# Performance work log

Measured on AMD Instinct MI355X. Metric: run time of the kernel, lower is better.

Reference implementation:

```python
import jax, jax.numpy as jnp
import numpy as np

N_NODES = 100000
N_EDGES = 3200000
N_GRAPHS = 64
NEG_SLOPE = 0.2


def mish(x):
    return x * jnp.tanh(jax.nn.softplus(x))


def gat_layer(x, src, dst, W, b, a_src, a_dst, heads, out_ch, n_nodes):
    # h: [N, H, C]
    h = (x @ W).reshape(n_nodes, heads, out_ch)
    alpha_s = jnp.sum(h * a_src[None], axis=-1)  # [N, H]
    alpha_d = jnp.sum(h * a_dst[None], axis=-1)  # [N, H]
    e = jax.nn.leaky_relu(alpha_s[src] + alpha_d[dst], NEG_SLOPE)  # [E, H]
    # scatter-softmax over incoming edges of each destination node
    emax = jax.ops.segment_max(e, dst, num_segments=n_nodes)  # [N, H]
    ee = jnp.exp(e - emax[dst])
    den = jax.ops.segment_sum(ee, dst, num_segments=n_nodes)
    alpha = ee / (den[dst] + 1e-16)  # [E, H]
    msg = h[src] * alpha[..., None]  # [E, H, C]
    out = jax.ops.segment_sum(msg, dst, num_segments=n_nodes)
    return out.reshape(n_nodes, heads * out_ch) + b


def setup_inputs() -> dict:
    key = jax.random.key(0)
    ks = jax.random.split(key, 10)
    x = jax.random.normal(ks[0], (N_NODES, 128), dtype=jnp.float32)
    edge_index = jax.random.randint(ks[1], (2, N_EDGES), 0, N_NODES, dtype=jnp.int64)
    batch = jnp.sort(jax.random.randint(ks[2], (N_NODES,), 0, N_GRAPHS, dtype=jnp.int64))
    s1 = 1.0 / np.sqrt(128.0)
    s2 = 1.0 / np.sqrt(16.0)
    return {
        "x": x,
        "edge_index": edge_index,
        "batch": batch,
        "W1": jax.random.normal(ks[3], (128, 16), dtype=jnp.float32) * s1,
        "b1": jnp.zeros((16,), dtype=jnp.float32),
        "a_src1": jax.random.normal(ks[4], (4, 4), dtype=jnp.float32) * 0.5,
        "a_dst1": jax.random.normal(ks[5], (4, 4), dtype=jnp.float32) * 0.5,
        "W2": jax.random.normal(ks[6], (16, 32), dtype=jnp.float32) * s2,
        "b2": jnp.zeros((32,), dtype=jnp.float32),
        "a_src2": jax.random.normal(ks[7], (1, 32), dtype=jnp.float32) * 0.5,
        "a_dst2": jax.random.normal(ks[8], (1, 32), dtype=jnp.float32) * 0.5,
    }


def reference(x, edge_index, batch, W1, b1, a_src1, a_dst1, W2, b2, a_src2, a_dst2):
    n = x.shape[0]
    # PyG GATConv default add_self_loops=True
    loop = jnp.arange(n, dtype=edge_index.dtype)
    src = jnp.concatenate([edge_index[0], loop])
    dst = jnp.concatenate([edge_index[1], loop])
    h = mish(gat_layer(x, src, dst, W1, b1, a_src1, a_dst1, heads=4, out_ch=4, n_nodes=n))
    h = mish(gat_layer(h, src, dst, W2, b2, a_src2, a_dst2, heads=1, out_ch=32, n_nodes=n))
    # global_mean_pool
    sums = jax.ops.segment_sum(h, batch, num_segments=N_GRAPHS)
    cnts = jax.ops.segment_sum(jnp.ones((n,), h.dtype), batch, num_segments=N_GRAPHS)
    return sums / jnp.maximum(cnts, 1.0)[:, None]
```

## Files before the change

kernel.cpp:

```cpp
#include <hip/hip_runtime.h>
#include <hip/hip_fp16.h>
#include <math.h>

#define NEG_SLOPE 0.2f
#define SB 256
#define NBMAX 1024
#define CAP 5120

typedef _Float16 half2v __attribute__((ext_vector_type(2)));

__device__ __forceinline__ float mishf(float x) {
    if (x > 15.f) return x;
    float ex = __expf(x);
    float y = 1.f + ex;
    float y2 = y * y;
    return x * (y2 - 1.f) / (y2 + 1.f);
}

__device__ __forceinline__ float lw(float e) {
    return __expf(fmaxf(e, NEG_SLOPE * e));
}

__device__ __forceinline__ float hdot2(half2v a, half2v b) {
#if __has_builtin(__builtin_amdgcn_fdot2)
    return __builtin_amdgcn_fdot2(a, b, 0.f, false);
#else
    return (float)a.x * (float)b.x + (float)a.y * (float)b.y;
#endif
}

__global__ void gemm1_kernel(const float* __restrict__ x, const float* __restrict__ W1,
                             const float* __restrict__ a_dst,
                             const float* __restrict__ W2, const float* __restrict__ as2,
                             const float* __restrict__ ad2,
                             _Float16* __restrict__ hpre1h, float* __restrict__ addst,
                             int* __restrict__ cursor, float* __restrict__ pool,
                             float* __restrict__ cnt, float* __restrict__ vs,
                             float* __restrict__ vd, int NB, int NG, int N) {
    __shared__ float Wl[128 * 16];
    __shared__ float xs[16 * 132];
    int tid = threadIdx.x;
    if (blockIdx.x == 0) {
        for (int i = tid; i < NB; i += 256) cursor[i] = 0;
        for (int i = tid; i < NG * 32; i += 256) pool[i] = 0.f;
        for (int i = tid; i < NG; i += 256) cnt[i] = 0.f;
        if (tid < 16) {
            float ps = 0.f, pd = 0.f;
            #pragma unroll
            for (int c = 0; c < 32; c++) {
                float w = W2[tid * 32 + c];
                ps += w * as2[c];
                pd += w * ad2[c];
            }
            vs[tid] = ps; vd[tid] = pd;
        }
    }
    for (int i = tid; i < 2048; i += 256) Wl[i] = W1[i];
    int nodebase = blockIdx.x * 16;
    const float4* x4 = (const float4*)(x + (size_t)nodebase * 128);
    for (int i = tid; i < 512; i += 256) {
        float4 v = x4[i];
        int e = i * 4;
        int nl = e >> 7, k = e & 127;
        float* dp = &xs[nl * 132 + k];
        dp[0] = v.x; dp[1] = v.y; dp[2] = v.z; dp[3] = v.w;
    }
    __syncthreads();
    int nl = tid >> 4, ch = tid & 15;
    const float* xr = &xs[nl * 132];
    float acc = 0.f;
    #pragma unroll 8
    for (int k = 0; k < 128; k++) acc += xr[k] * Wl[k * 16 + ch];
    int node = nodebase + nl;
    if (node < N) {
        hpre1h[node * 16 + ch] = (_Float16)acc;
        float pd = acc * a_dst[ch];
        pd += __shfl_xor(pd, 1); pd += __shfl_xor(pd, 2);
        if ((ch & 3) == 0) addst[node * 4 + (ch >> 2)] = pd;
    }
}

__global__ __launch_bounds__(1024) void scatF_kernel(
        const int* __restrict__ src, const int* __restrict__ dst,
        int E, int Etot, int CH, int NB,
        int* __restrict__ cursor, int* __restrict__ pairs) {
    __shared__ int lcnt[NBMAX];
    __shared__ int lbase[NBMAX];
    int tid = threadIdx.x, blk = blockIdx.x;
    for (int b = tid; b < NB; b += 1024) lcnt[b] = 0;
    __syncthreads();
    int ibeg = blk * CH, iend = min((blk + 1) * CH, Etot);
    for (int i = ibeg + tid; i < iend; i += 1024) {
        int d = (i < E) ? dst[i] : (i - E);
        atomicAdd(&lcnt[d >> 7], 1);
    }
    __syncthreads();
    for (int b = tid; b < NB; b += 1024) {
        int h = lcnt[b];
        lbase[b] = h ? atomicAdd(&cursor[b], h) : 0;
    }
    __syncthreads();
    for (int b = tid; b < NB; b += 1024) lcnt[b] = 0;
    __syncthreads();
    for (int i = ibeg + tid; i < iend; i += 1024) {
        int s, d;
        if (i < E) { s = src[i]; d = dst[i]; } else { s = d = i - E; }
        int b = d >> 7, dl = d & 127;
        int r = atomicAdd(&lcnt[b], 1);
        int pos = lbase[b] + r;
        pairs[(size_t)b * CAP + (pos < CAP ? pos : CAP - 1)] = s | (dl << 17);
    }
}

__global__ __launch_bounds__(1024) void csragg1_kernel(
        const int* __restrict__ pairs, const int* __restrict__ btotal,
        int NB, int N,
        int* __restrict__ ssorted, int* __restrict__ rs, int* __restrict__ re,
        const float* __restrict__ a_src1, const float* __restrict__ addst,
        const _Float16* __restrict__ hpre1h, const float* __restrict__ b1,
        const float* __restrict__ vs, const float* __restrict__ vd,
        _Float16* __restrict__ hpost1h,
        float* __restrict__ as2n, float* __restrict__ ad2n) {
    __shared__ int deg[128];
    __shared__ int s[128];
    __shared__ int cur[128];
    int tid = threadIdx.x, b = blockIdx.x;
    int nb0 = b << 7;
    int cnt_nodes = min(128, N - nb0);
    int bstart = b * CAP;
    int bend = bstart + btotal[b];
    if (tid < 128) deg[tid] = 0;
    __syncthreads();
    for (int j = bstart + tid; j < bend; j += 1024)
        atomicAdd(&deg[(pairs[j] >> 17) & 127], 1);
    __syncthreads();
    if (tid < 128) s[tid] = deg[tid];
    __syncthreads();
    for (int o = 1; o < 128; o <<= 1) {
        int v = 0;
        if (tid < 128 && tid >= o) v = s[tid - o];
        __syncthreads();
        if (tid < 128) s[tid] += v;
        __syncthreads();
    }
    if (tid < 128) {
        int ex = bstart + s[tid] - deg[tid];
        cur[tid] = ex;
        if (tid < cnt_nodes) {
            rs[nb0 + tid] = ex;
            re[nb0 + tid] = ex + deg[tid];
        }
    }
    __syncthreads();
    for (int j = bstart + tid; j < bend; j += 1024) {
        int p = pairs[j];
        int pos = atomicAdd(&cur[(p >> 17) & 127], 1);
        ssorted[pos] = p & 0x1FFFF;
    }
    __syncthreads();

    int wave = tid >> 6;
    int lane = tid & 63;
    int er = lane >> 3, hc = lane & 7, head = hc >> 1;
    int c0 = hc * 2;
    half2v wsh;
    wsh.x = (_Float16)a_src1[c0];
    wsh.y = (_Float16)a_src1[c0 + 1];
    const _Float16* hb = hpre1h + c0;
    for (int r = 0; r < 8; r++) {
        int ln = (wave << 3) + r;
        if (ln >= cnt_nodes) break;
        int node = nb0 + ln;
        int end = cur[ln];
        int start = end - deg[ln];
        float adh = addst[node * 4 + head];
        float den = 0.f, a0 = 0.f, a1 = 0.f;
        int last = end - 1;
        int jb = start;
        for (; jb + 16 <= end; jb += 16) {
            int j0 = jb + er, j1 = j0 + 8;
            int s0 = ssorted[j0];
            int s1 = ssorted[j1];
            half2v h0 = *(const half2v*)(hb + s0 * 16);
            half2v h1 = *(const half2v*)(hb + s1 * 16);
            float p0 = hdot2(h0, wsh);
            float p1 = hdot2(h1, wsh);
            float w0 = lw(p0 + __shfl_xor(p0, 1) + adh);
            float w1 = lw(p1 + __shfl_xor(p1, 1) + adh);
            den += w0 + w1;
            a0 += (float)h0.x * w0 + (float)h1.x * w1;
            a1 += (float)h0.y * w0 + (float)h1.y * w1;
        }
        if (jb < end) {
            int j0 = jb + er, j1 = j0 + 8;
            int k0 = (j0 <= last) ? j0 : last;
            int k1 = (j1 <= last) ? j1 : last;
            int s0 = ssorted[k0];
            int s1 = ssorted[k1];
            half2v h0 = *(const half2v*)(hb + s0 * 16);
            half2v h1 = *(const half2v*)(hb + s1 * 16);
            float p0 = hdot2(h0, wsh);
            float p1 = hdot2(h1, wsh);
            float e0 = p0 + __shfl_xor(p0, 1) + adh;
            float e1 = p1 + __shfl_xor(p1, 1) + adh;
            float w0 = (j0 <= last) ? lw(e0) : 0.f;
            float w1 = (j1 <= last) ? lw(e1) : 0.f;
            den += w0 + w1;
            a0 += (float)h0.x * w0 + (float)h1.x * w1;
            a1 += (float)h0.y * w0 + (float)h1.y * w1;
        }
        a0 += __shfl_xor(a0, 8);  a1 += __shfl_xor(a1, 8);  den += __shfl_xor(den, 8);
        a0 += __shfl_xor(a0, 16); a1 += __shfl_xor(a1, 16); den += __shfl_xor(den, 16);
        a0 += __shfl_xor(a0, 32); a1 += __shfl_xor(a1, 32); den += __shfl_xor(den, 32);
        if (er == 0) {
            float inv = 1.f / (den + 1e-16f);
            float o0 = mishf(a0 * inv + b1[c0]);
            float o1 = mishf(a1 * inv + b1[c0 + 1]);
            half2v oh;
            oh.x = (_Float16)o0; oh.y = (_Float16)o1;
            *(half2v*)(hpost1h + node * 16 + c0) = oh;
            float ps = o0 * vs[c0] + o1 * vs[c0 + 1];
            float pd = o0 * vd[c0] + o1 * vd[c0 + 1];
            ps += __shfl_xor(ps, 1); pd += __shfl_xor(pd, 1);
            ps += __shfl_xor(ps, 2); pd += __shfl_xor(pd, 2);
            ps += __shfl_xor(ps, 4); pd += __shfl_xor(pd, 4);
            if (hc == 0) { as2n[node] = ps; ad2n[node] = pd; }
        }
    }
}

__global__ void agg2_kernel(const int* __restrict__ rs, const int* __restrict__ re,
                            const int* __restrict__ ssorted,
                            const float* __restrict__ as2n, const float* __restrict__ ad2n,
                            const _Float16* __restrict__ hpost1h,
                            float* __restrict__ agg16, float* __restrict__ denv, int N) {
    int wave = threadIdx.x >> 6;
    int lane = threadIdx.x & 63;
    int node = blockIdx.x * 4 + wave;
    if (node >= N) return;
    int start = rs[node], end = re[node];
    int er = lane >> 3, hc = lane & 7;
    int c0 = hc * 2;
    float adh = ad2n[node];
    const _Float16* hb = hpost1h + c0;
    float den = 0.f, a0 = 0.f, a1 = 0.f;
    int last = end - 1;
    int jb = start;
    for (; jb + 16 <= end; jb += 16) {
        int j0 = jb + er, j1 = j0 + 8;
        int s0 = __builtin_nontemporal_load(ssorted + j0);
        int s1 = __builtin_nontemporal_load(ssorted + j1);
        float e0 = as2n[s0] + adh;
        float e1 = as2n[s1] + adh;
        half2v h0 = *(const half2v*)(hb + s0 * 16);
        half2v h1 = *(const half2v*)(hb + s1 * 16);
        float w0 = lw(e0);
        float w1 = lw(e1);
        den += w0 + w1;
        a0 += (float)h0.x * w0 + (float)h1.x * w1;
        a1 += (float)h0.y * w0 + (float)h1.y * w1;
    }
    if (jb < end) {
        int j0 = jb + er, j1 = j0 + 8;
        int k0 = (j0 <= last) ? j0 : last;
        int k1 = (j1 <= last) ? j1 : last;
        int s0 = __builtin_nontemporal_load(ssorted + k0);
        int s1 = __builtin_nontemporal_load(ssorted + k1);
        float e0 = as2n[s0] + adh;
        float e1 = as2n[s1] + adh;
        half2v h0 = *(const half2v*)(hb + s0 * 16);
        half2v h1 = *(const half2v*)(hb + s1 * 16);
        float w0 = (j0 <= last) ? lw(e0) : 0.f;
        float w1 = (j1 <= last) ? lw(e1) : 0.f;
        den += w0 + w1;
        a0 += (float)h0.x * w0 + (float)h1.x * w1;
        a1 += (float)h0.y * w0 + (float)h1.y * w1;
    }
    a0 += __shfl_xor(a0, 8);  a1 += __shfl_xor(a1, 8);  den += __shfl_xor(den, 8);
    a0 += __shfl_xor(a0, 16); a1 += __shfl_xor(a1, 16); den += __shfl_xor(den, 16);
    a0 += __shfl_xor(a0, 32); a1 += __shfl_xor(a1, 32); den += __shfl_xor(den, 32);
    if (er == 0) {
        float2 o; o.x = a0; o.y = a1;
        *(float2*)(agg16 + node * 16 + c0) = o;
        if (hc == 0) denv[node] = den;
    }
}

__global__ void post2pool_kernel(const float* __restrict__ agg16, const float* __restrict__ denv,
                                 const float* __restrict__ W2, const float* __restrict__ b2,
                                 const int* __restrict__ batch,
                                 float* __restrict__ pool, float* __restrict__ cnt, int N) {
    __shared__ float Wl[16 * 32];
    int tid = threadIdx.x;
    for (int i = tid; i < 512; i += 256) Wl[i] = W2[i];
    __syncthreads();
    int r = tid >> 5, ch = tid & 31;
    float bc = b2[ch];
    int base = blockIdx.x * 512;
    int cur = -1;
    float sum = 0.f, c = 0.f;
    for (int it = 0; it < 64; it++) {
        int n = base + it * 8 + r;
        if (n >= N) break;
        int g = batch[n];
        if (g != cur) {
            if (cur >= 0) {
                atomicAdd(&pool[cur * 32 + ch], sum);
                if (ch == 0) atomicAdd(&cnt[cur], c);
            }
            cur = g; sum = 0.f; c = 0.f;
        }
        const float* ar = agg16 + (size_t)n * 16;
        float acc = 0.f;
        #pragma unroll
        for (int k = 0; k < 16; k++) acc += ar[k] * Wl[k * 32 + ch];
        float val = mishf(acc / (denv[n] + 1e-16f) + bc);
        sum += val;
        c += 1.f;
    }
    if (cur >= 0) {
        atomicAdd(&pool[cur * 32 + ch], sum);
        if (ch == 0) atomicAdd(&cnt[cur], c);
    }
}

__global__ void fin_kernel(const float* __restrict__ pool, const float* __restrict__ cnt,
                           float* __restrict__ out, int NG) {
    int i = blockIdx.x * blockDim.x + threadIdx.x;
    if (i >= NG * 32) return;
    out[i] = pool[i] / fmaxf(cnt[i >> 5], 1.0f);
}

extern "C" void kernel_launch(void* const* d_in, const int* in_sizes, int n_in,
                              void* d_out, int out_size, void* d_ws, size_t ws_size,
                              hipStream_t stream) {
    const float* x   = (const float*)d_in[0];
    const int* eidx  = (const int*)d_in[1];
    const int* batch = (const int*)d_in[2];
    const float* W1  = (const float*)d_in[3];
    const float* b1  = (const float*)d_in[4];
    const float* as1 = (const float*)d_in[5];
    const float* ad1 = (const float*)d_in[6];
    const float* W2  = (const float*)d_in[7];
    const float* b2  = (const float*)d_in[8];
    const float* as2 = (const float*)d_in[9];
    const float* ad2 = (const float*)d_in[10];
    float* out = (float*)d_out;

    int N = in_sizes[0] / 128;
    int E = in_sizes[1] / 2;
    int Etot = E + N;
    int NG = out_size / 32;
    const int* esrc = eidx;
    const int* edst = eidx + E;

    int NB = (N + 127) >> 7;
    int CH = (Etot + SB - 1) / SB;

    char* p = (char*)d_ws;
    auto alloc = [&](size_t nbytes) {
        p = (char*)(((uintptr_t)p + 15) & ~(uintptr_t)15);
        void* r = (void*)p; p += nbytes; return r;
    };
    int* pairs        = (int*)alloc((size_t)NB * CAP * 4);
    int* ssorted      = (int*)alloc((size_t)NB * CAP * 4);
    int* rs           = (int*)alloc((size_t)N * 4);
    int* re           = (int*)alloc((size_t)N * 4);
    int* cursor       = (int*)alloc((size_t)NB * 4);
    _Float16* hpre1h  = (_Float16*)alloc((size_t)N * 16 * 2);
    _Float16* hpost1h = (_Float16*)alloc((size_t)N * 16 * 2);
    float* addst1  = (float*)alloc((size_t)N * 4 * 4);
    float* as2n    = (float*)alloc((size_t)N * 4);
    float* ad2n    = (float*)alloc((size_t)N * 4);
    float* agg16   = (float*)alloc((size_t)N * 16 * 4);
    float* denv    = (float*)alloc((size_t)N * 4);
    float* vs      = (float*)alloc(16 * 4);
    float* vd      = (float*)alloc(16 * 4);
    float* pool    = (float*)alloc((size_t)NG * 32 * 4);
    float* cnt     = (float*)alloc((size_t)NG * 4);

    gemm1_kernel<<<(N + 15) / 16, 256, 0, stream>>>(x, W1, ad1, W2, as2, ad2,
                                                    hpre1h, addst1, cursor, pool, cnt,
                                                    vs, vd, NB, NG, N);
    scatF_kernel<<<SB, 1024, 0, stream>>>(esrc, edst, E, Etot, CH, NB, cursor, pairs);
    csragg1_kernel<<<NB, 1024, 0, stream>>>(pairs, cursor, NB, N,
                                            ssorted, rs, re, as1, addst1, hpre1h,
                                            b1, vs, vd, hpost1h, as2n, ad2n);
    agg2_kernel<<<(N + 3) / 4, 256, 0, stream>>>(rs, re, ssorted, as2n, ad2n, hpost1h,
                                                 agg16, denv, N);
    post2pool_kernel<<<(N + 511) / 512, 256, 0, stream>>>(agg16, denv, W2, b2, batch,
                                                          pool, cnt, N);
    fin_kernel<<<(NG * 32 + 255) / 256, 256, 0, stream>>>(pool, cnt, out, NG);
}
```

Baseline: 349.9 us.

## Merge GEMM1 and edge bucketing into one launch; stage sorted sources in LDS

Combines the layer-1 projection GEMM and the edge bucket-scatter into a single kernel whose blocks are split by block index, so the two independent stages can run concurrently. The scatter moves from 256 blocks of 1024 threads to 1024 blocks of 256. Zeroing of cursor, pool and count buffers moves to a single hipMemsetAsync over contiguously allocated buffers. The CSR aggregation kernel now keeps the per-bucket sorted source list in shared memory and reads it from there during aggregation, which adds 20 KB of LDS per block and may reduce occupancy.

```diff
diff --git a/kernel.cpp b/kernel.cpp
--- a/kernel.cpp
+++ b/kernel.cpp
@@ -3,7 +3,7 @@
 #include <math.h>
 
 #define NEG_SLOPE 0.2f
-#define SB 256
+#define SCB 1024
 #define NBMAX 1024
 #define CAP 5120
 
@@ -29,22 +29,50 @@
 #endif
 }
 
-__global__ void gemm1_kernel(const float* __restrict__ x, const float* __restrict__ W1,
-                             const float* __restrict__ a_dst,
-                             const float* __restrict__ W2, const float* __restrict__ as2,
-                             const float* __restrict__ ad2,
-                             _Float16* __restrict__ hpre1h, float* __restrict__ addst,
-                             int* __restrict__ cursor, float* __restrict__ pool,
-                             float* __restrict__ cnt, float* __restrict__ vs,
-                             float* __restrict__ vd, int NB, int NG, int N) {
-    __shared__ float Wl[128 * 16];
-    __shared__ float xs[16 * 132];
+__global__ __launch_bounds__(256) void gemm1scat_kernel(
+        const float* __restrict__ x, const float* __restrict__ W1,
+        const float* __restrict__ a_dst,
+        const float* __restrict__ W2, const float* __restrict__ as2,
+        const float* __restrict__ ad2,
+        _Float16* __restrict__ hpre1h, float* __restrict__ addst,
+        const int* __restrict__ src, const int* __restrict__ dst,
+        int E, int Etot, int CH, int NB,
+        int* __restrict__ cursor, int* __restrict__ pairs,
+        float* __restrict__ vs, float* __restrict__ vd,
+        int G1, int N) {
+    __shared__ char smem[16640];
     int tid = threadIdx.x;
-    if (blockIdx.x == 0) {
-        for (int i = tid; i < NB; i += 256) cursor[i] = 0;
-        for (int i = tid; i < NG * 32; i += 256) pool[i] = 0.f;
-        for (int i = tid; i < NG; i += 256) cnt[i] = 0.f;
-        if (tid < 16) {
+    if ((int)blockIdx.x < G1) {
+        float* Wl = (float*)smem;
+        float* xs = (float*)(smem + 8192);
+        for (int i = tid; i < 2048; i += 256) Wl[i] = W1[i];
+        int nodebase = blockIdx.x * 16;
+        const float4* x4 = (const float4*)(x + (size_t)nodebase * 128);
+        for (int i = tid; i < 512; i += 256) {
+            float4 v = x4[i];
+            int e = i * 4;
+            int nl = e >> 7, k = e & 127;
+            float* dp = &xs[nl * 132 + k];
+            dp[0] = v.x; dp[1] = v.y; dp[2] = v.z; dp[3] = v.w;
+        }
+        __syncthreads();
+        int nl = tid >> 4, ch = tid & 15;
+        const float* xr = &xs[nl * 132];
+        float acc = 0.f;
+        #pragma unroll 8
+        for (int k = 0; k < 128; k++) acc += xr[k] * Wl[k * 16 + ch];
+        int node = nodebase + nl;
+        if (node < N) {
+            hpre1h[node * 16 + ch] = (_Float16)acc;
+            float pd = acc * a_dst[ch];
+            pd += __shfl_xor(pd, 1); pd += __shfl_xor(pd, 2);
+            if ((ch & 3) == 0) addst[node * 4 + (ch >> 2)] = pd;
+        }
+    } else {
+        int* lcnt  = (int*)smem;
+        int* lbase = (int*)(smem + 4096);
+        int blk = blockIdx.x - G1;
+        if (blk == 0 && tid < 16) {
             float ps = 0.f, pd = 0.f;
             #pragma unroll
             for (int c = 0; c < 32; c++) {
@@ -54,61 +82,29 @@
             }
             vs[tid] = ps; vd[tid] = pd;
         }
-    }
-    for (int i = tid; i < 2048; i += 256) Wl[i] = W1[i];
-    int nodebase = blockIdx.x * 16;
-    const float4* x4 = (const float4*)(x + (size_t)nodebase * 128);
-    for (int i = tid; i < 512; i += 256) {
-        float4 v = x4[i];
-        int e = i * 4;
-        int nl = e >> 7, k = e & 127;
-        float* dp = &xs[nl * 132 + k];
-        dp[0] = v.x; dp[1] = v.y; dp[2] = v.z; dp[3] = v.w;
-    }
-    __syncthreads();
-    int nl = tid >> 4, ch = tid & 15;
-    const float* xr = &xs[nl * 132];
-    float acc = 0.f;
-    #pragma unroll 8
-    for (int k = 0; k < 128; k++) acc += xr[k] * Wl[k * 16 + ch];
-    int node = nodebase + nl;
-    if (node < N) {
-        hpre1h[node * 16 + ch] = (_Float16)acc;
-        float pd = acc * a_dst[ch];
-        pd += __shfl_xor(pd, 1); pd += __shfl_xor(pd, 2);
-        if ((ch & 3) == 0) addst[node * 4 + (ch >> 2)] = pd;
-    }
-}
-
-__global__ __launch_bounds__(1024) void scatF_kernel(
-        const int* __restrict__ src, const int* __restrict__ dst,
-        int E, int Etot, int CH, int NB,
-        int* __restrict__ cursor, int* __restrict__ pairs) {
-    __shared__ int lcnt[NBMAX];
-    __shared__ int lbase[NBMAX];
-    int tid = threadIdx.x, blk = blockIdx.x;
-    for (int b = tid; b < NB; b += 1024) lcnt[b] = 0;
-    __syncthreads();
-    int ibeg = blk * CH, iend = min((blk + 1) * CH, Etot);
-    for (int i = ibeg + tid; i < iend; i += 1024) {
-        int d = (i < E) ? dst[i] : (i - E);
-        atomicAdd(&lcnt[d >> 7], 1);
-    }
-    __syncthreads();
-    for (int b = tid; b < NB; b += 1024) {
-        int h = lcnt[b];
-        lbase[b] = h ? atomicAdd(&cursor[b], h) : 0;
-    }
-    __syncthreads();
-    for (int b = tid; b < NB; b += 1024) lcnt[b] = 0;
-    __syncthreads();
-    for (int i = ibeg + tid; i < iend; i += 1024) {
-        int s, d;
-        if (i < E) { s = src[i]; d = dst[i]; } else { s = d = i - E; }
-        int b = d >> 7, dl = d & 127;
-        int r = atomicAdd(&lcnt[b], 1);
-        int pos = lbase[b] + r;
-        pairs[(size_t)b * CAP + (pos < CAP ? pos : CAP - 1)] = s | (dl << 17);
+        for (int b = tid; b < NB; b += 256) lcnt[b] = 0;
+        __syncthreads();
+        int ibeg = blk * CH, iend = min((blk + 1) * CH, Etot);
+        for (int i = ibeg + tid; i < iend; i += 256) {
+            int d = (i < E) ? dst[i] : (i - E);
+            atomicAdd(&lcnt[d >> 7], 1);
+        }
+        __syncthreads();
+        for (int b = tid; b < NB; b += 256) {
+            int h = lcnt[b];
+            lbase[b] = h ? atomicAdd(&cursor[b], h) : 0;
+        }
+        __syncthreads();
+        for (int b = tid; b < NB; b += 256) lcnt[b] = 0;
+        __syncthreads();
+        for (int i = ibeg + tid; i < iend; i += 256) {
+            int s, d;
+            if (i < E) { s = src[i]; d = dst[i]; } else { s = d = i - E; }
+            int b = d >> 7, dl = d & 127;
+            int r = atomicAdd(&lcnt[b], 1);
+            int pos = lbase[b] + r;
+            pairs[(size_t)b * CAP + (pos < CAP ? pos : CAP - 1)] = s | (dl << 17);
+        }
     }
 }
 
@@ -124,15 +120,16 @@
     __shared__ int deg[128];
     __shared__ int s[128];
     __shared__ int cur[128];
+    __shared__ int lss[CAP];
     int tid = threadIdx.x, b = blockIdx.x;
     int nb0 = b << 7;
     int cnt_nodes = min(128, N - nb0);
     int bstart = b * CAP;
-    int bend = bstart + btotal[b];
+    int total = min(btotal[b], CAP);
     if (tid < 128) deg[tid] = 0;
     __syncthreads();
-    for (int j = bstart + tid; j < bend; j += 1024)
-        atomicAdd(&deg[(pairs[j] >> 17) & 127], 1);
+    for (int j = tid; j < total; j += 1024)
+        atomicAdd(&deg[(pairs[bstart + j] >> 17) & 127], 1);
     __syncthreads();
     if (tid < 128) s[tid] = deg[tid];
     __syncthreads();
@@ -144,20 +141,21 @@
         __syncthreads();
     }
     if (tid < 128) {
-        int ex = bstart + s[tid] - deg[tid];
-        cur[tid] = ex;
+        cur[tid] = s[tid] - deg[tid];
         if (tid < cnt_nodes) {
-            rs[nb0 + tid] = ex;
-            re[nb0 + tid] = ex + deg[tid];
-        }
-    }
-    __syncthreads();
-    for (int j = bstart + tid; j < bend; j += 1024) {
-        int p = pairs[j];
+            rs[nb0 + tid] = bstart + s[tid] - deg[tid];
+            re[nb0 + tid] = bstart + s[tid];
+        }
+    }
+    __syncthreads();
+    for (int j = tid; j < total; j += 1024) {
+        int p = pairs[bstart + j];
         int pos = atomicAdd(&cur[(p >> 17) & 127], 1);
-        ssorted[pos] = p & 0x1FFFF;
-    }
-    __syncthreads();
+        lss[pos] = p & 0x1FFFF;
+    }
+    __syncthreads();
+    for (int j = tid; j < total; j += 1024)
+        ssorted[bstart + j] = lss[j];
 
     int wave = tid >> 6;
     int lane = tid & 63;
@@ -179,8 +177,8 @@
         int jb = start;
         for (; jb + 16 <= end; jb += 16) {
             int j0 = jb + er, j1 = j0 + 8;
-            int s0 = ssorted[j0];
-            int s1 = ssorted[j1];
+            int s0 = lss[j0];
+            int s1 = lss[j1];
             half2v h0 = *(const half2v*)(hb + s0 * 16);
             half2v h1 = *(const half2v*)(hb + s1 * 16);
             float p0 = hdot2(h0, wsh);
@@ -195,8 +193,8 @@
             int j0 = jb + er, j1 = j0 + 8;
             int k0 = (j0 <= last) ? j0 : last;
             int k1 = (j1 <= last) ? j1 : last;
-            int s0 = ssorted[k0];
-            int s1 = ssorted[k1];
+            int s0 = lss[k0];
+            int s1 = lss[k1];
             half2v h0 = *(const half2v*)(hb + s0 * 16);
             half2v h1 = *(const half2v*)(hb + s1 * 16);
             float p0 = hdot2(h0, wsh);
@@ -355,7 +353,8 @@
     const int* edst = eidx + E;
 
     int NB = (N + 127) >> 7;
-    int CH = (Etot + SB - 1) / SB;
+    int CH = (Etot + SCB - 1) / SCB;
+    int G1 = (N + 15) / 16;
 
     char* p = (char*)d_ws;
     auto alloc = [&](size_t nbytes) {
@@ -367,6 +366,8 @@
     int* rs           = (int*)alloc((size_t)N * 4);
     int* re           = (int*)alloc((size_t)N * 4);
     int* cursor       = (int*)alloc((size_t)NB * 4);
+    float* pool       = (float*)alloc((size_t)NG * 32 * 4);
+    float* cnt        = (float*)alloc((size_t)NG * 4);
     _Float16* hpre1h  = (_Float16*)alloc((size_t)N * 16 * 2);
     _Float16* hpost1h = (_Float16*)alloc((size_t)N * 16 * 2);
     float* addst1  = (float*)alloc((size_t)N * 4 * 4);
@@ -376,13 +377,13 @@
     float* denv    = (float*)alloc((size_t)N * 4);
     float* vs      = (float*)alloc(16 * 4);
     float* vd      = (float*)alloc(16 * 4);
-    float* pool    = (float*)alloc((size_t)NG * 32 * 4);
-    float* cnt     = (float*)alloc((size_t)NG * 4);
-
-    gemm1_kernel<<<(N + 15) / 16, 256, 0, stream>>>(x, W1, ad1, W2, as2, ad2,
-                                                    hpre1h, addst1, cursor, pool, cnt,
-                                                    vs, vd, NB, NG, N);
-    scatF_kernel<<<SB, 1024, 0, stream>>>(esrc, edst, E, Etot, CH, NB, cursor, pairs);
+
+    hipMemsetAsync(cursor, 0, (size_t)(NB + NG * 32 + NG) * 4, stream);
+
+    gemm1scat_kernel<<<G1 + SCB, 256, 0, stream>>>(x, W1, ad1, W2, as2, ad2,
+                                                   hpre1h, addst1, esrc, edst,
+                                                   E, Etot, CH, NB, cursor, pairs,
+                                                   vs, vd, G1, N);
     csragg1_kernel<<<NB, 1024, 0, stream>>>(pairs, cursor, NB, N,
                                             ssorted, rs, re, as1, addst1, hpre1h,
                                             b1, vs, vd, hpost1h, as2n, ad2n);
```

Measured after the change: 358.4 us. +2.4%, slower.
